# Kernel optimization log

Measured on AMD Instinct MI355X. Metric: run time of the kernel, lower is better.

## Reference

```python
import jax, jax.numpy as jnp
import numpy as np

N_NODES = 50000
N_EDGES = 800000
F_IN = 128
HIDDEN = 128
N_CLASSES = 10
N_GRAPHS = 256


def _glorot(key, shape):
    lim = float(np.sqrt(6.0 / (shape[0] + shape[1])))
    return jax.random.uniform(key, shape, jnp.float32, -lim, lim)


def setup_inputs() -> dict:
    key = jax.random.key(0)
    ks = jax.random.split(key, 12)
    x = jax.random.normal(ks[0], (N_NODES, F_IN), jnp.float32)
    edge_index = jax.random.randint(ks[1], (2, N_EDGES), 0, N_NODES, jnp.int64)
    batch = jnp.sort(jax.random.randint(ks[2], (N_NODES,), 0, N_GRAPHS, jnp.int64))
    dims = [(F_IN, HIDDEN), (HIDDEN, HIDDEN), (HIDDEN, N_CLASSES)]
    params = {}
    for i, (din, dout) in enumerate(dims, start=1):
        params[f"Wl{i}"] = _glorot(ks[2 + 2 * i], (din, dout))   # lin_l: applied to aggregated neighbors (has bias)
        params[f"bl{i}"] = jnp.zeros((dout,), jnp.float32)
        params[f"Wr{i}"] = _glorot(ks[3 + 2 * i], (din, dout))   # lin_r: applied to root/self features (no bias)
    return {"x": x, "edge_index": edge_index, "batch": batch, **params}


def _sage_conv(x, src, dst, Wl, bl, Wr):
    # mean aggregation of source features at destination nodes
    msg = x[src]                                                    # [E, D] gather
    ssum = jax.ops.segment_sum(msg, dst, num_segments=N_NODES)      # [N, D]
    cnt = jax.ops.segment_sum(jnp.ones((src.shape[0],), x.dtype), dst, num_segments=N_NODES)
    agg = ssum / jnp.maximum(cnt, 1.0)[:, None]
    return agg @ Wl + bl + x @ Wr


def reference(x, edge_index, batch, Wl1, bl1, Wr1, Wl2, bl2, Wr2, Wl3, bl3, Wr3):
    src, dst = edge_index[0], edge_index[1]
    h = _sage_conv(x, src, dst, Wl1, bl1, Wr1)
    h = _sage_conv(h, src, dst, Wl2, bl2, Wr2)
    h = _sage_conv(h, src, dst, Wl3, bl3, Wr3)                      # [N, C]
    # global mean pool over graphs
    gsum = jax.ops.segment_sum(h, batch, num_segments=N_GRAPHS)     # [G, C]
    gcnt = jax.ops.segment_sum(jnp.ones((h.shape[0],), h.dtype), batch, num_segments=N_GRAPHS)
    pooled = gsum / jnp.maximum(gcnt, 1.0)[:, None]
    return jax.nn.log_softmax(pooled, axis=-1)
```

## Files before the change

kernel.cpp:

```cpp
#include <hip/hip_runtime.h>


#define CAP 48
#define EB 4096

typedef __attribute__((ext_vector_type(8))) short short8;
typedef __attribute__((ext_vector_type(4))) float floatx4;

static __device__ __forceinline__ unsigned short f2bf(float f) {
    unsigned int u = __float_as_uint(f);
    u += 0x7FFFu + ((u >> 16) & 1u);
    return (unsigned short)(u >> 16);
}
static __device__ __forceinline__ float bf2f(unsigned short b) {
    return __uint_as_float(((unsigned int)b) << 16);
}
static __device__ __forceinline__ unsigned int packbf2(float a, float b) {
    return (unsigned int)f2bf(a) | ((unsigned int)f2bf(b) << 16);
}

__global__ void prep1(const int* __restrict__ ei, int E, int ablk, int nbk, int N,
                      unsigned int* __restrict__ bedges, int* __restrict__ runCnt,
                      const float* __restrict__ Wl2, const float* __restrict__ Wr2,
                      const float* __restrict__ Wl3, const float* __restrict__ Wr3,
                      float* __restrict__ m2Mg,
                      int* __restrict__ zero_base, int zero_words,
                      unsigned int* __restrict__ y3z, unsigned int* __restrict__ u1z,
                      unsigned int* __restrict__ u2w) {
    __shared__ int hist[512];
    __shared__ float wtT_s[128 * 20];
    if (blockIdx.x < (unsigned)ablk) {
        for (int i = threadIdx.x; i < nbk; i += 256) hist[i] = 0;
        __syncthreads();
        int e0 = blockIdx.x * EB + threadIdx.x;
        unsigned int pk[16];
        int bk[16], loc[16];
#pragma unroll
        for (int k = 0; k < 16; ++k) {
            int e = e0 + k * 256;
            if (e < E) {
                int src = ei[e];
                int dst = ei[E + e];
                bk[k] = dst >> 7;
                pk[k] = ((unsigned int)(dst & 127) << 16) | (unsigned int)src;
                loc[k] = atomicAdd(&hist[bk[k]], 1);
            } else bk[k] = -1;
        }
        __syncthreads();
        for (int i = threadIdx.x; i < nbk; i += 256)
            runCnt[(size_t)blockIdx.x * nbk + i] = hist[i];
#pragma unroll
        for (int k = 0; k < 16; ++k)
            if (bk[k] >= 0 && loc[k] < CAP)
                bedges[((size_t)bk[k] * ablk + blockIdx.x) * CAP + loc[k]] = pk[k];
        return;
    }
    int rb = blockIdx.x - ablk;
    if (rb < 4) {
        const int tid = threadIdx.x;
        for (int i = tid; i < 2560; i += 256) {
            int f = i / 20, c = i - f * 20;
            wtT_s[i] = (c < 10) ? Wl3[f * 10 + c] : Wr3[f * 10 + (c - 10)];
        }
        __syncthreads();
        int jl = tid >> 3;
        int cg = tid & 7;
        int j = rb * 32 + jl;
        const float* w2row = ((cg < 4) ? Wl2 : Wr2) + (size_t)j * 128;
        int c20 = (cg & 3) * 5;
        float acc[5] = {0.f, 0.f, 0.f, 0.f, 0.f};
        for (int f4 = 0; f4 < 32; ++f4) {
            float4 wv = *(const float4*)&w2row[f4 * 4];
#pragma unroll
            for (int e = 0; e < 4; ++e) {
                float w = (e == 0) ? wv.x : (e == 1) ? wv.y : (e == 2) ? wv.z : wv.w;
                const float* wt = &wtT_s[(f4 * 4 + e) * 20 + c20];
#pragma unroll
                for (int i = 0; i < 5; ++i) acc[i] += w * wt[i];
            }
        }
        int cc = (cg >> 2) * 20 + c20;
#pragma unroll
        for (int i = 0; i < 5; ++i) m2Mg[j * 40 + cc + i] = acc[i];
        return;
    }
    if (rb == 4) {
        if (threadIdx.x < 6)  y3z[(size_t)N * 6 + threadIdx.x] = 0;
        if (threadIdx.x >= 32 && threadIdx.x < 38)
            u1z[(size_t)N * 6 + (threadIdx.x - 32)] = 0;
        if (threadIdx.x >= 64 && threadIdx.x < 70)
            u2w[(size_t)N * 6 + (threadIdx.x - 64)] = 0;
        return;
    }
    int i = (rb - 5) * 256 + threadIdx.x;
    if (i < zero_words) zero_base[i] = 0;
}

__global__ __launch_bounds__(256) void prep2(
    const float* __restrict__ Wl1, const float* __restrict__ Wr1,
    const float* __restrict__ Wl3, const float* __restrict__ Wr3,
    const float* __restrict__ bl1, const float* __restrict__ bl2,
    const float* __restrict__ bl3,
    const float* __restrict__ m2Mg, short* __restrict__ Wq,
    float* __restrict__ cbv) {
    __shared__ float m2s[128 * 40];
    __shared__ float aLR[32][80];
    const int tid = threadIdx.x;
    if (blockIdx.x == 4) {
        for (int i = tid; i < 3072; i += 256) {
            int k = i & 127;
            int t = i >> 7;
            int mt = t / 6, m = 10 + t % 6;
            int ks = k >> 5, rem = k & 31, qq = rem >> 3, jj = rem & 7;
            int l = qq * 16 + m;
            Wq[(((mt * 4 + ks) * 64) + l) * 8 + jj] = 0;
        }
        if (tid < 30) {
            float s = 0.f;
            if (tid < 10) {
                int c = tid;
                for (int k = 0; k < 128; ++k) s += bl1[k] * m2Mg[k * 40 + c];
            } else if (tid < 20) {
                int c = tid - 10;
                for (int k = 0; k < 128; ++k)
                    s += bl1[k] * (m2Mg[k * 40 + 20 + c] + m2Mg[k * 40 + 10 + c]);
                for (int f = 0; f < 128; ++f) s += bl2[f] * Wl3[f * 10 + c];
            } else {
                int c = tid - 20;
                for (int k = 0; k < 128; ++k) s += bl1[k] * m2Mg[k * 40 + 30 + c];
                for (int f = 0; f < 128; ++f) s += bl2[f] * Wr3[f * 10 + c];
                s += bl3[c];
            }
            cbv[tid] = s;
        }
        return;
    }
    for (int i = tid; i < 5120; i += 256) m2s[i] = m2Mg[i];
    __syncthreads();
    int kl = tid >> 3;
    int cg = tid & 7;
    int k = blockIdx.x * 32 + kl;
    int c0 = cg * 5;
    const float* wl = Wl1 + (size_t)k * 128;
    const float* wr = Wr1 + (size_t)k * 128;
    float accL[5] = {0.f, 0.f, 0.f, 0.f, 0.f};
    float accR[5] = {0.f, 0.f, 0.f, 0.f, 0.f};
    for (int j4 = 0; j4 < 32; ++j4) {
        float4 wa = *(const float4*)&wl[j4 * 4];
        float4 wb = *(const float4*)&wr[j4 * 4];
#pragma unroll
        for (int e = 0; e < 4; ++e) {
            float wle = (e == 0) ? wa.x : (e == 1) ? wa.y : (e == 2) ? wa.z : wa.w;
            float wre = (e == 0) ? wb.x : (e == 1) ? wb.y : (e == 2) ? wb.z : wb.w;
            const float* mr = &m2s[(j4 * 4 + e) * 40 + c0];
#pragma unroll
            for (int i = 0; i < 5; ++i) {
                accL[i] += wle * mr[i];
                accR[i] += wre * mr[i];
            }
        }
    }
#pragma unroll
    for (int i = 0; i < 5; ++i) {
        aLR[kl][c0 + i] = accL[i];
        aLR[kl][40 + c0 + i] = accR[i];
    }
    __syncthreads();
    int ks = k >> 5, rem = k & 31, qq = rem >> 3, jj = rem & 7;
#pragma unroll
    for (int i = 0; i < 5; ++i) {
        int f = c0 + i;
        float val;
        if (f < 10) {
            val = aLR[kl][f];
        } else if (f < 20) {
            int c = f - 10;
            val = aLR[kl][40 + c] + aLR[kl][20 + c] + aLR[kl][10 + c];
        } else if (f < 30) {
            int c = f - 20;
            val = aLR[kl][40 + 10 + c] + aLR[kl][40 + 20 + c] + aLR[kl][30 + c];
        } else {
            int c = f - 30;
            val = aLR[kl][40 + 30 + c];
        }
        int mt = f / 10, c = f % 10;
        int l = qq * 16 + c;
        Wq[(((mt * 4 + ks) * 64) + l) * 8 + jj] = (short)f2bf(val);
    }
}

__global__ __launch_bounds__(256) void fillX(
    const float* __restrict__ x, const short* __restrict__ Wq,
    unsigned short* __restrict__ y3, float* __restrict__ yS, int N,
    int nbk, int ablk,
    const unsigned int* __restrict__ bedges, const int* __restrict__ runCnt,
    int* __restrict__ cnt, unsigned short* __restrict__ colbuf) {
    __shared__ unsigned short As[64 * 136];
    __shared__ int lcnt[128];
    if (blockIdx.x >= (unsigned)nbk) {
        int blk = blockIdx.x - nbk;
        int node0 = blk * 64;
#pragma unroll
        for (int c = 0; c < 8; ++c) {
            int idx = c * 256 + threadIdx.x;
            int r = idx >> 5;
            int c4 = idx & 31;
            int row = node0 + r;
            float4 v = make_float4(0.f, 0.f, 0.f, 0.f);
            if (row < N) v = *(const float4*)&x[(size_t)row * 128 + c4 * 4];
            ushort4 p;
            p.x = f2bf(v.x); p.y = f2bf(v.y); p.z = f2bf(v.z); p.w = f2bf(v.w);
            *(ushort4*)&As[r * 136 + c4 * 4] = p;
        }
        __syncthreads();

        const int w = threadIdx.x >> 6;
        const int lane = threadIdx.x & 63;
        const int q = lane >> 4;
        const int m = lane & 15;

        floatx4 acc[4] = {};
#pragma unroll
        for (int s = 0; s < 4; ++s) {
            short8 bfrag = *(const short8*)&As[(w * 16 + m) * 136 + s * 32 + q * 8];
#pragma unroll
            for (int mi = 0; mi < 4; ++mi) {
                short8 wf = *(const short8*)&Wq[((mi * 4 + s) * 64 + lane) * 8];
                acc[mi] = __builtin_amdgcn_mfma_f32_16x16x32_bf16(
                    wf, bfrag, acc[mi], 0, 0, 0);
            }
        }
        int node = node0 + w * 16 + m;
        if (node < N) {
            int l = q * 4;
            {
                floatx4 a = acc[0];
                if (l < 8) {
                    ushort4 p;
                    p.x = f2bf(a[0]); p.y = f2bf(a[1]);
                    p.z = f2bf(a[2]); p.w = f2bf(a[3]);
                    *(ushort4*)&y3[(size_t)node * 12 + l] = p;
                } else if (l == 8) {
                    ushort2 p2;
                    p2.x = f2bf(a[0]); p2.y = f2bf(a[1]);
                    *(ushort2*)&y3[(size_t)node * 12 + 8] = p2;
                }
            }
#pragma unroll
            for (int mi = 1; mi < 4; ++mi) {
                floatx4 a = acc[mi];
                size_t off = (size_t)node * 36 + (mi - 1) * 12 + l;
                if (l < 8) {
                    *(float4*)&yS[off] = make_float4(a[0], a[1], a[2], a[3]);
                } else if (l == 8) {
                    *(float2*)&yS[off] = make_float2(a[0], a[1]);
                }
            }
        }
    } else {
        int b = blockIdx.x;
        if (threadIdx.x < 128) lcnt[threadIdx.x] = 0;
        __syncthreads();
        for (int blk = threadIdx.x; blk < ablk; blk += 256) {
            int c = runCnt[(size_t)blk * nbk + b];
            c = min(c, CAP);
            size_t ebase = ((size_t)b * ablk + blk) * CAP;
            for (int i = 0; i < c; ++i) {
                unsigned int pk = bedges[ebase + i];
                int dl = pk >> 16;
                int slot = atomicAdd(&lcnt[dl], 1);
                if (slot < CAP)
                    colbuf[(size_t)(b * 128 + dl) * CAP + slot] =
                        (unsigned short)(pk & 0xFFFFu);
            }
        }
        __syncthreads();
        int node = b * 128 + threadIdx.x;
        if (threadIdx.x < 128 && node < N) cnt[node] = lcnt[threadIdx.x];
    }
}

__global__ __launch_bounds__(256) void g1(
    const unsigned int* __restrict__ y3z, const int* __restrict__ cnt,
    const unsigned short* __restrict__ colbuf, const float2* __restrict__ yS2,
    unsigned int* __restrict__ u1z, int N) {
    const int lane = threadIdx.x & 63;
    const int wvi = threadIdx.x >> 6;
    const int la = lane & 15;
    const int qb = lane & 48;
    const int node = blockIdx.x * 16 + wvi * 4 + (lane >> 4);
    const bool valid = node < N;
    const int nodec = valid ? node : N - 1;
    const int deg = cnt[nodec];
    const int d = valid ? min(deg, CAP) : 0;
    const unsigned short* cb = colbuf + (size_t)nodec * CAP;
    const int sub = (la < 5) ? la : la - 5;

    float f0 = 0.f, f1 = 0.f;
    int nb = (d + 15) >> 4;
    for (int b = 0; b < nb; ++b) {
        int slot = b * 16 + la;
        int idx = (slot < d) ? (int)cb[slot] : N;
        unsigned int vv[8];
#pragma unroll
        for (int j = 0; j < 8; ++j) {
            int s0 = __shfl(idx, qb + 2 * j, 64);
            int s1 = __shfl(idx, qb + 2 * j + 1, 64);
            int sr = (la < 5) ? s0 : s1;
            vv[j] = (la < 10) ? y3z[(size_t)sr * 6 + sub] : 0u;
        }
#pragma unroll
        for (int j = 0; j < 8; ++j) {
            f0 += bf2f((unsigned short)(vv[j] & 0xFFFF));
            f1 += bf2f((unsigned short)(vv[j] >> 16));
        }
    }
    int pl = (la < 5) ? (lane + 5) : (lane - 5);
    f0 += __shfl(f0, pl, 64);
    f1 += __shfl(f1, pl, 64);
    if (valid && la < 5) {
        float inv = 1.0f / (float)max(deg, 1);
        float2 sv = yS2[(size_t)node * 18 + la];
        u1z[(size_t)node * 6 + la] = packbf2(f0 * inv + sv.x, f1 * inv + sv.y);
    }
}

__global__ __launch_bounds__(256) void g2(
    const unsigned int* __restrict__ u1z, const int* __restrict__ cnt,
    const unsigned short* __restrict__ colbuf, const float2* __restrict__ yS2,
    const float2* __restrict__ cbv2, unsigned int* __restrict__ u2w, int N) {
    const int lane = threadIdx.x & 63;
    const int wvi = threadIdx.x >> 6;
    const int la = lane & 15;
    const int qb = lane & 48;
    const int node = blockIdx.x * 16 + wvi * 4 + (lane >> 4);
    const bool valid = node < N;
    const int nodec = valid ? node : N - 1;
    const int deg = cnt[nodec];
    const int d = valid ? min(deg, CAP) : 0;
    const unsigned short* cb = colbuf + (size_t)nodec * CAP;
    const int sub = (la < 5) ? la : la - 5;

    float f0 = 0.f, f1 = 0.f;
    int nb = (d + 15) >> 4;
    for (int b = 0; b < nb; ++b) {
        int slot = b * 16 + la;
        int idx = (slot < d) ? (int)cb[slot] : N;
        unsigned int vv[8];
#pragma unroll
        for (int j = 0; j < 8; ++j) {
            int s0 = __shfl(idx, qb + 2 * j, 64);
            int s1 = __shfl(idx, qb + 2 * j + 1, 64);
            int sr = (la < 5) ? s0 : s1;
            vv[j] = (la < 10) ? u1z[(size_t)sr * 6 + sub] : 0u;
        }
#pragma unroll
        for (int j = 0; j < 8; ++j) {
            f0 += bf2f((unsigned short)(vv[j] & 0xFFFF));
            f1 += bf2f((unsigned short)(vv[j] >> 16));
        }
    }
    int pl = (la < 5) ? (lane + 5) : (lane - 5);
    f0 += __shfl(f0, pl, 64);
    f1 += __shfl(f1, pl, 64);
    if (valid && la < 5) {
        float inv = 1.0f / (float)max(deg, 1);
        float2 sv = yS2[(size_t)node * 18 + 6 + la];
        float2 v1 = cbv2[la];
        float b0 = sv.x + ((deg > 0) ? v1.x : 0.f);
        float b1 = sv.y + ((deg > 0) ? v1.y : 0.f);
        u2w[(size_t)node * 6 + la] = packbf2(f0 * inv + b0, f1 * inv + b1);
    }
}

__global__ __launch_bounds__(256) void g3pool(
    const unsigned int* __restrict__ u2w, const int* __restrict__ cnt,
    const unsigned short* __restrict__ colbuf, const float2* __restrict__ yS2,
    const float2* __restrict__ cbv2, const int* __restrict__ batch,
    float* __restrict__ gsum, float* __restrict__ gcnt, int N) {
    __shared__ float ls[2816];
    for (int i = threadIdx.x; i < 2816; i += 256) ls[i] = 0.f;
    __syncthreads();

    const int lane = threadIdx.x & 63;
    const int wvi = threadIdx.x >> 6;
    const int la = lane & 15;
    const int qb = lane & 48;
    const int node = blockIdx.x * 16 + wvi * 4 + (lane >> 4);
    const bool valid = node < N;
    const int nodec = valid ? node : N - 1;
    const int deg = cnt[nodec];
    const int d = valid ? min(deg, CAP) : 0;
    const unsigned short* cb = colbuf + (size_t)nodec * CAP;
    const int sub = (la < 5) ? la : la - 5;

    float f0 = 0.f, f1 = 0.f;
    int nb = (d + 15) >> 4;
    for (int b = 0; b < nb; ++b) {
        int slot = b * 16 + la;
        int idx = (slot < d) ? (int)cb[slot] : N;
        unsigned int vv[8];
#pragma unroll
        for (int j = 0; j < 8; ++j) {
            int s0 = __shfl(idx, qb + 2 * j, 64);
            int s1 = __shfl(idx, qb + 2 * j + 1, 64);
            int sr = (la < 5) ? s0 : s1;
            vv[j] = (la < 10) ? u2w[(size_t)sr * 6 + sub] : 0u;
        }
#pragma unroll
        for (int j = 0; j < 8; ++j) {
            f0 += bf2f((unsigned short)(vv[j] & 0xFFFF));
            f1 += bf2f((unsigned short)(vv[j] >> 16));
        }
    }
    int pl = (la < 5) ? (lane + 5) : (lane - 5);
    f0 += __shfl(f0, pl, 64);
    f1 += __shfl(f1, pl, 64);
    if (valid && la < 5) {
        float inv = 1.0f / (float)max(deg, 1);
        float2 y0 = yS2[(size_t)node * 18 + 12 + la];
        float2 v0 = cbv2[5 + la];
        float2 vc = cbv2[10 + la];
        float h0 = f0 * inv + y0.x + ((deg > 0) ? v0.x : 0.f) + vc.x;
        float h1 = f1 * inv + y0.y + ((deg > 0) ? v0.y : 0.f) + vc.y;
        int g = batch[node];
        atomicAdd(&ls[g * 10 + 2 * la], h0);
        atomicAdd(&ls[g * 10 + 2 * la + 1], h1);
        if (la == 0) atomicAdd(&ls[2560 + g], 1.0f);
    }
    __syncthreads();
    for (int i = threadIdx.x; i < 2816; i += 256) {
        float v = ls[i];
        if (v != 0.f) {
            if (i < 2560) atomicAdd(&gsum[i], v);
            else          atomicAdd(&gcnt[i - 2560], v);
        }
    }
}

__global__ void finalize_pool(const float* __restrict__ gsum,
                              const float* __restrict__ gcnt,
                              float* __restrict__ out, int G) {
    int g = blockIdx.x * blockDim.x + threadIdx.x;
    if (g >= G) return;
    float inv = 1.0f / fmaxf(gcnt[g], 1.0f);
    float p[10];
    float m = -1e30f;
#pragma unroll
    for (int c = 0; c < 10; ++c) { p[c] = gsum[g * 10 + c] * inv; m = fmaxf(m, p[c]); }
    float s = 0.f;
#pragma unroll
    for (int c = 0; c < 10; ++c) s += expf(p[c] - m);
    float lse = logf(s);
#pragma unroll
    for (int c = 0; c < 10; ++c) out[g * 10 + c] = p[c] - m - lse;
}

extern "C" void kernel_launch(void* const* d_in, const int* in_sizes, int n_in,
                              void* d_out, int out_size, void* d_ws, size_t ws_size,
                              hipStream_t stream) {
    const float* x    = (const float*)d_in[0];
    const int*   ei   = (const int*)d_in[1];
    const int*   batch= (const int*)d_in[2];
    const float* Wl1  = (const float*)d_in[3];
    const float* bl1  = (const float*)d_in[4];
    const float* Wr1  = (const float*)d_in[5];
    const float* Wl2  = (const float*)d_in[6];
    const float* bl2  = (const float*)d_in[7];
    const float* Wr2  = (const float*)d_in[8];
    const float* Wl3  = (const float*)d_in[9];
    const float* bl3  = (const float*)d_in[10];
    const float* Wr3  = (const float*)d_in[11];
    float* out = (float*)d_out;

    const int N = in_sizes[2];
    const int E = in_sizes[1] / 2;
    const int G = out_size / 10;
    const int ablk = (E + EB - 1) / EB;
    const int nbk  = (N + 127) >> 7;

    char* ws = (char*)d_ws;
    size_t o = 0;
    float* gsum   = (float*)(ws + o); o += (size_t)G * 10 * 4;
    float* gcnt   = (float*)(ws + o); o += (size_t)G * 4;
    size_t zero_bytes = (o + 255) & ~(size_t)255;
    o = zero_bytes;
    int*            cnt    = (int*)(ws + o);            o += (size_t)N * 4;
    unsigned short* colbuf = (unsigned short*)(ws + o); o += ((size_t)N * CAP * 2 + 255) & ~(size_t)255;
    short*          Wq     = (short*)(ws + o);          o += (size_t)8192 * 2;
    float*          cbv    = (float*)(ws + o);          o += 32 * 4;
    o = (o + 255) & ~(size_t)255;
    float*          m2Mg   = (float*)(ws + o);          o += (size_t)128 * 40 * 4;
    o = (o + 255) & ~(size_t)255;
    unsigned short* y3t    = (unsigned short*)(ws + o); o += (size_t)(N + 1) * 12 * 2;
    o = (o + 255) & ~(size_t)255;
    float*          yS     = (float*)(ws + o);          o += (size_t)N * 36 * 4;
    unsigned short* u1z    = (unsigned short*)(ws + o); o += (size_t)(N + 1) * 12 * 2;
    o = (o + 255) & ~(size_t)255;
    unsigned short* u2w    = (unsigned short*)(ws + o); o += (size_t)(N + 1) * 12 * 2;
    o = (o + 255) & ~(size_t)255;
    unsigned int*   bedges = (unsigned int*)(ws + o);   o += (size_t)nbk * ablk * CAP * 4;
    int*            runCnt = (int*)(ws + o);            o += (size_t)ablk * nbk * 4;

    int zero_words = (int)(zero_bytes / 4);
    int zblocks = (zero_words + 255) / 256;
    prep1<<<ablk + 5 + zblocks, 256, 0, stream>>>(
        ei, E, ablk, nbk, N, bedges, runCnt,
        Wl2, Wr2, Wl3, Wr3, m2Mg,
        (int*)ws, zero_words,
        (unsigned int*)y3t, (unsigned int*)u1z, (unsigned int*)u2w);

    prep2<<<5, 256, 0, stream>>>(Wl1, Wr1, Wl3, Wr3, bl1, bl2, bl3,
                                 m2Mg, Wq, cbv);

    int gblocks = (N + 63) / 64;
    int ablocks = (N + 15) / 16;
    fillX<<<nbk + gblocks, 256, 0, stream>>>(x, Wq, y3t, yS, N,
                                             nbk, ablk, bedges, runCnt,
                                             cnt, colbuf);

    g1<<<ablocks, 256, 0, stream>>>((const unsigned int*)y3t, cnt, colbuf,
                                    (const float2*)yS, (unsigned int*)u1z, N);
    g2<<<ablocks, 256, 0, stream>>>((const unsigned int*)u1z, cnt, colbuf,
                                    (const float2*)yS, (const float2*)cbv,
                                    (unsigned int*)u2w, N);
    g3pool<<<ablocks, 256, 0, stream>>>((const unsigned int*)u2w, cnt, colbuf,
                                        (const float2*)yS, (const float2*)cbv,
                                        batch, gsum, gcnt, N);
    finalize_pool<<<1, 256, 0, stream>>>(gsum, gcnt, out, G);
}
```

Measured before the change: 170.0 us.

## Pad gathered bf16 rows to 16 elements and gather 8-byte chunks per lane

The per-node bf16 tables y3/u1/u2 are padded from 12 to 16 shorts (32 bytes), so each neighbour row is read as three uint2 loads. The gather loop now processes 4 neighbours per 16-lane group instead of 2 and reduces with xor shuffles. The loop over neighbours is fully unrolled over the CAP slots, with a per-chunk degree guard. This cuts the number of gather iterations and shuffles per edge, at the cost of 33% more table storage and padded writes in the producer and in the bias vector layout.

```diff
diff --git a/kernel.cpp b/kernel.cpp
--- a/kernel.cpp
+++ b/kernel.cpp
@@ -85,11 +85,11 @@
         return;
     }
     if (rb == 4) {
-        if (threadIdx.x < 6)  y3z[(size_t)N * 6 + threadIdx.x] = 0;
-        if (threadIdx.x >= 32 && threadIdx.x < 38)
-            u1z[(size_t)N * 6 + (threadIdx.x - 32)] = 0;
-        if (threadIdx.x >= 64 && threadIdx.x < 70)
-            u2w[(size_t)N * 6 + (threadIdx.x - 64)] = 0;
+        if (threadIdx.x < 8)  y3z[(size_t)N * 8 + threadIdx.x] = 0;
+        if (threadIdx.x >= 32 && threadIdx.x < 40)
+            u1z[(size_t)N * 8 + (threadIdx.x - 32)] = 0;
+        if (threadIdx.x >= 64 && threadIdx.x < 72)
+            u2w[(size_t)N * 8 + (threadIdx.x - 64)] = 0;
         return;
     }
     int i = (rb - 5) * 256 + threadIdx.x;
@@ -115,21 +115,22 @@
             int l = qq * 16 + m;
             Wq[(((mt * 4 + ks) * 64) + l) * 8 + jj] = 0;
         }
-        if (tid < 30) {
+        if (tid < 48) {
+            int grp = tid >> 4;
+            int c = tid & 15;
             float s = 0.f;
-            if (tid < 10) {
-                int c = tid;
-                for (int k = 0; k < 128; ++k) s += bl1[k] * m2Mg[k * 40 + c];
-            } else if (tid < 20) {
-                int c = tid - 10;
-                for (int k = 0; k < 128; ++k)
-                    s += bl1[k] * (m2Mg[k * 40 + 20 + c] + m2Mg[k * 40 + 10 + c]);
-                for (int f = 0; f < 128; ++f) s += bl2[f] * Wl3[f * 10 + c];
-            } else {
-                int c = tid - 20;
-                for (int k = 0; k < 128; ++k) s += bl1[k] * m2Mg[k * 40 + 30 + c];
-                for (int f = 0; f < 128; ++f) s += bl2[f] * Wr3[f * 10 + c];
-                s += bl3[c];
+            if (c < 10) {
+                if (grp == 0) {
+                    for (int k = 0; k < 128; ++k) s += bl1[k] * m2Mg[k * 40 + c];
+                } else if (grp == 1) {
+                    for (int k = 0; k < 128; ++k)
+                        s += bl1[k] * (m2Mg[k * 40 + 20 + c] + m2Mg[k * 40 + 10 + c]);
+                    for (int f = 0; f < 128; ++f) s += bl2[f] * Wl3[f * 10 + c];
+                } else {
+                    for (int k = 0; k < 128; ++k) s += bl1[k] * m2Mg[k * 40 + 30 + c];
+                    for (int f = 0; f < 128; ++f) s += bl2[f] * Wr3[f * 10 + c];
+                    s += bl3[c];
+                }
             }
             cbv[tid] = s;
         }
@@ -235,16 +236,10 @@
             int l = q * 4;
             {
                 floatx4 a = acc[0];
-                if (l < 8) {
-                    ushort4 p;
-                    p.x = f2bf(a[0]); p.y = f2bf(a[1]);
-                    p.z = f2bf(a[2]); p.w = f2bf(a[3]);
-                    *(ushort4*)&y3[(size_t)node * 12 + l] = p;
-                } else if (l == 8) {
-                    ushort2 p2;
-                    p2.x = f2bf(a[0]); p2.y = f2bf(a[1]);
-                    *(ushort2*)&y3[(size_t)node * 12 + 8] = p2;
-                }
+                ushort4 p;
+                p.x = f2bf(a[0]); p.y = f2bf(a[1]);
+                p.z = f2bf(a[2]); p.w = f2bf(a[3]);
+                *(ushort4*)&y3[(size_t)node * 16 + l] = p;
             }
 #pragma unroll
             for (int mi = 1; mi < 4; ++mi) {
@@ -253,7 +248,7 @@
                 if (l < 8) {
                     *(float4*)&yS[off] = make_float4(a[0], a[1], a[2], a[3]);
                 } else if (l == 8) {
-                    *(float2*)&yS[off] = make_float2(a[0], a[1]);
+                    *(float4*)&yS[off] = make_float4(a[0], a[1], a[2], a[3]);
                 }
             }
         }
@@ -280,103 +275,126 @@
     }
 }
 
+
 __global__ __launch_bounds__(256) void g1(
-    const unsigned int* __restrict__ y3z, const int* __restrict__ cnt,
-    const unsigned short* __restrict__ colbuf, const float2* __restrict__ yS2,
-    unsigned int* __restrict__ u1z, int N) {
+    const uint2* __restrict__ tbl, const int* __restrict__ cnt,
+    const unsigned short* __restrict__ colbuf, const float4* __restrict__ ySq,
+    uint2* __restrict__ outt, int N) {
     const int lane = threadIdx.x & 63;
     const int wvi = threadIdx.x >> 6;
     const int la = lane & 15;
     const int qb = lane & 48;
+    const int e = la >> 2;
+    const int p = la & 3;
     const int node = blockIdx.x * 16 + wvi * 4 + (lane >> 4);
     const bool valid = node < N;
     const int nodec = valid ? node : N - 1;
     const int deg = cnt[nodec];
     const int d = valid ? min(deg, CAP) : 0;
     const unsigned short* cb = colbuf + (size_t)nodec * CAP;
-    const int sub = (la < 5) ? la : la - 5;
-
-    float f0 = 0.f, f1 = 0.f;
-    int nb = (d + 15) >> 4;
-    for (int b = 0; b < nb; ++b) {
-        int slot = b * 16 + la;
-        int idx = (slot < d) ? (int)cb[slot] : N;
-        unsigned int vv[8];
-#pragma unroll
-        for (int j = 0; j < 8; ++j) {
-            int s0 = __shfl(idx, qb + 2 * j, 64);
-            int s1 = __shfl(idx, qb + 2 * j + 1, 64);
-            int sr = (la < 5) ? s0 : s1;
-            vv[j] = (la < 10) ? y3z[(size_t)sr * 6 + sub] : 0u;
-        }
-#pragma unroll
-        for (int j = 0; j < 8; ++j) {
-            f0 += bf2f((unsigned short)(vv[j] & 0xFFFF));
-            f1 += bf2f((unsigned short)(vv[j] >> 16));
-        }
-    }
-    int pl = (la < 5) ? (lane + 5) : (lane - 5);
-    f0 += __shfl(f0, pl, 64);
-    f1 += __shfl(f1, pl, 64);
-    if (valid && la < 5) {
-        float inv = 1.0f / (float)max(deg, 1);
-        float2 sv = yS2[(size_t)node * 18 + la];
-        u1z[(size_t)node * 6 + la] = packbf2(f0 * inv + sv.x, f1 * inv + sv.y);
+
+    int i0 = (la < d) ? (int)cb[la] : N;
+    int i1 = (16 + la < d) ? (int)cb[16 + la] : N;
+    int i2 = (32 + la < d) ? (int)cb[32 + la] : N;
+
+    float a0 = 0.f, a1 = 0.f, a2 = 0.f, a3 = 0.f;
+#pragma unroll
+    for (int k = 0; k < 3; ++k) {
+        int cur = (k == 0) ? i0 : ((k == 1) ? i1 : i2);
+#pragma unroll
+        for (int tt = 0; tt < 4; ++tt) {
+            int base = k * 16 + tt * 4;
+            if (base < d) {
+                int s = __shfl(cur, qb + tt * 4 + e, 64);
+                uint2 v = make_uint2(0u, 0u);
+                if (p < 3) v = tbl[(size_t)s * 4 + p];
+                a0 += bf2f((unsigned short)(v.x & 0xFFFF));
+                a1 += bf2f((unsigned short)(v.x >> 16));
+                a2 += bf2f((unsigned short)(v.y & 0xFFFF));
+                a3 += bf2f((unsigned short)(v.y >> 16));
+            }
+        }
+    }
+    a0 += __shfl_xor(a0, 4, 64); a0 += __shfl_xor(a0, 8, 64);
+    a1 += __shfl_xor(a1, 4, 64); a1 += __shfl_xor(a1, 8, 64);
+    a2 += __shfl_xor(a2, 4, 64); a2 += __shfl_xor(a2, 8, 64);
+    a3 += __shfl_xor(a3, 4, 64); a3 += __shfl_xor(a3, 8, 64);
+    if (valid && la < 4) {
+        uint2 o = make_uint2(0u, 0u);
+        if (la < 3) {
+            float inv = 1.0f / (float)max(deg, 1);
+            float4 sv = ySq[(size_t)node * 9 + la];
+            o.x = packbf2(a0 * inv + sv.x, a1 * inv + sv.y);
+            o.y = packbf2(a2 * inv + sv.z, a3 * inv + sv.w);
+        }
+        outt[(size_t)node * 4 + la] = o;
     }
 }
 
 __global__ __launch_bounds__(256) void g2(
-    const unsigned int* __restrict__ u1z, const int* __restrict__ cnt,
-    const unsigned short* __restrict__ colbuf, const float2* __restrict__ yS2,
-    const float2* __restrict__ cbv2, unsigned int* __restrict__ u2w, int N) {
+    const uint2* __restrict__ tbl, const int* __restrict__ cnt,
+    const unsigned short* __restrict__ colbuf, const float4* __restrict__ ySq,
+    const float* __restrict__ cbv, uint2* __restrict__ outt, int N) {
     const int lane = threadIdx.x & 63;
     const int wvi = threadIdx.x >> 6;
     const int la = lane & 15;
     const int qb = lane & 48;
+    const int e = la >> 2;
+    const int p = la & 3;
     const int node = blockIdx.x * 16 + wvi * 4 + (lane >> 4);
     const bool valid = node < N;
     const int nodec = valid ? node : N - 1;
     const int deg = cnt[nodec];
     const int d = valid ? min(deg, CAP) : 0;
     const unsigned short* cb = colbuf + (size_t)nodec * CAP;
-    const int sub = (la < 5) ? la : la - 5;
-
-    float f0 = 0.f, f1 = 0.f;
-    int nb = (d + 15) >> 4;
-    for (int b = 0; b < nb; ++b) {
-        int slot = b * 16 + la;
-        int idx = (slot < d) ? (int)cb[slot] : N;
-        unsigned int vv[8];
-#pragma unroll
-        for (int j = 0; j < 8; ++j) {
-            int s0 = __shfl(idx, qb + 2 * j, 64);
-            int s1 = __shfl(idx, qb + 2 * j + 1, 64);
-            int sr = (la < 5) ? s0 : s1;
-            vv[j] = (la < 10) ? u1z[(size_t)sr * 6 + sub] : 0u;
-        }
-#pragma unroll
-        for (int j = 0; j < 8; ++j) {
-            f0 += bf2f((unsigned short)(vv[j] & 0xFFFF));
-            f1 += bf2f((unsigned short)(vv[j] >> 16));
-        }
-    }
-    int pl = (la < 5) ? (lane + 5) : (lane - 5);
-    f0 += __shfl(f0, pl, 64);
-    f1 += __shfl(f1, pl, 64);
-    if (valid && la < 5) {
-        float inv = 1.0f / (float)max(deg, 1);
-        float2 sv = yS2[(size_t)node * 18 + 6 + la];
-        float2 v1 = cbv2[la];
-        float b0 = sv.x + ((deg > 0) ? v1.x : 0.f);
-        float b1 = sv.y + ((deg > 0) ? v1.y : 0.f);
-        u2w[(size_t)node * 6 + la] = packbf2(f0 * inv + b0, f1 * inv + b1);
+
+    int i0 = (la < d) ? (int)cb[la] : N;
+    int i1 = (16 + la < d) ? (int)cb[16 + la] : N;
+    int i2 = (32 + la < d) ? (int)cb[32 + la] : N;
+
+    float a0 = 0.f, a1 = 0.f, a2 = 0.f, a3 = 0.f;
+#pragma unroll
+    for (int k = 0; k < 3; ++k) {
+        int cur = (k == 0) ? i0 : ((k == 1) ? i1 : i2);
+#pragma unroll
+        for (int tt = 0; tt < 4; ++tt) {
+            int base = k * 16 + tt * 4;
+            if (base < d) {
+                int s = __shfl(cur, qb + tt * 4 + e, 64);
+                uint2 v = make_uint2(0u, 0u);
+                if (p < 3) v = tbl[(size_t)s * 4 + p];
+                a0 += bf2f((unsigned short)(v.x & 0xFFFF));
+                a1 += bf2f((unsigned short)(v.x >> 16));
+                a2 += bf2f((unsigned short)(v.y & 0xFFFF));
+                a3 += bf2f((unsigned short)(v.y >> 16));
+            }
+        }
+    }
+    a0 += __shfl_xor(a0, 4, 64); a0 += __shfl_xor(a0, 8, 64);
+    a1 += __shfl_xor(a1, 4, 64); a1 += __shfl_xor(a1, 8, 64);
+    a2 += __shfl_xor(a2, 4, 64); a2 += __shfl_xor(a2, 8, 64);
+    a3 += __shfl_xor(a3, 4, 64); a3 += __shfl_xor(a3, 8, 64);
+    if (valid && la < 4) {
+        uint2 o = make_uint2(0u, 0u);
+        if (la < 3) {
+            float inv = 1.0f / (float)max(deg, 1);
+            float4 sv = ySq[(size_t)node * 9 + 3 + la];
+            float4 v1 = *(const float4*)&cbv[la * 4];
+            float b0 = sv.x + ((deg > 0) ? v1.x : 0.f);
+            float b1 = sv.y + ((deg > 0) ? v1.y : 0.f);
+            float b2 = sv.z + ((deg > 0) ? v1.z : 0.f);
+            float b3 = sv.w + ((deg > 0) ? v1.w : 0.f);
+            o.x = packbf2(a0 * inv + b0, a1 * inv + b1);
+            o.y = packbf2(a2 * inv + b2, a3 * inv + b3);
+        }
+        outt[(size_t)node * 4 + la] = o;
     }
 }
 
 __global__ __launch_bounds__(256) void g3pool(
-    const unsigned int* __restrict__ u2w, const int* __restrict__ cnt,
-    const unsigned short* __restrict__ colbuf, const float2* __restrict__ yS2,
-    const float2* __restrict__ cbv2, const int* __restrict__ batch,
+    const uint2* __restrict__ tbl, const int* __restrict__ cnt,
+    const unsigned short* __restrict__ colbuf, const float4* __restrict__ ySq,
+    const float* __restrict__ cbv, const int* __restrict__ batch,
     float* __restrict__ gsum, float* __restrict__ gcnt, int N) {
     __shared__ float ls[2816];
     for (int i = threadIdx.x; i < 2816; i += 256) ls[i] = 0.f;
@@ -386,46 +404,58 @@
     const int wvi = threadIdx.x >> 6;
     const int la = lane & 15;
     const int qb = lane & 48;
+    const int e = la >> 2;
+    const int p = la & 3;
     const int node = blockIdx.x * 16 + wvi * 4 + (lane >> 4);
     const bool valid = node < N;
     const int nodec = valid ? node : N - 1;
     const int deg = cnt[nodec];
     const int d = valid ? min(deg, CAP) : 0;
     const unsigned short* cb = colbuf + (size_t)nodec * CAP;
-    const int sub = (la < 5) ? la : la - 5;
-
-    float f0 = 0.f, f1 = 0.f;
-    int nb = (d + 15) >> 4;
-    for (int b = 0; b < nb; ++b) {
-        int slot = b * 16 + la;
-        int idx = (slot < d) ? (int)cb[slot] : N;
-        unsigned int vv[8];
-#pragma unroll
-        for (int j = 0; j < 8; ++j) {
-            int s0 = __shfl(idx, qb + 2 * j, 64);
-            int s1 = __shfl(idx, qb + 2 * j + 1, 64);
-            int sr = (la < 5) ? s0 : s1;
-            vv[j] = (la < 10) ? u2w[(size_t)sr * 6 + sub] : 0u;
-        }
-#pragma unroll
-        for (int j = 0; j < 8; ++j) {
-            f0 += bf2f((unsigned short)(vv[j] & 0xFFFF));
-            f1 += bf2f((unsigned short)(vv[j] >> 16));
-        }
-    }
-    int pl = (la < 5) ? (lane + 5) : (lane - 5);
-    f0 += __shfl(f0, pl, 64);
-    f1 += __shfl(f1, pl, 64);
-    if (valid && la < 5) {
+
+    int i0 = (la < d) ? (int)cb[la] : N;
+    int i1 = (16 + la < d) ? (int)cb[16 + la] : N;
+    int i2 = (32 + la < d) ? (int)cb[32 + la] : N;
+
+    float a0 = 0.f, a1 = 0.f, a2 = 0.f, a3 = 0.f;
+#pragma unroll
+    for (int k = 0; k < 3; ++k) {
+        int cur = (k == 0) ? i0 : ((k == 1) ? i1 : i2);
+#pragma unroll
+        for (int tt = 0; tt < 4; ++tt) {
+            int base = k * 16 + tt * 4;
+            if (base < d) {
+                int s = __shfl(cur, qb + tt * 4 + e, 64);
+                uint2 v = make_uint2(0u, 0u);
+                if (p < 3) v = tbl[(size_t)s * 4 + p];
+                a0 += bf2f((unsigned short)(v.x & 0xFFFF));
+                a1 += bf2f((unsigned short)(v.x >> 16));
+                a2 += bf2f((unsigned short)(v.y & 0xFFFF));
+                a3 += bf2f((unsigned short)(v.y >> 16));
+            }
+        }
+    }
+    a0 += __shfl_xor(a0, 4, 64); a0 += __shfl_xor(a0, 8, 64);
+    a1 += __shfl_xor(a1, 4, 64); a1 += __shfl_xor(a1, 8, 64);
+    a2 += __shfl_xor(a2, 4, 64); a2 += __shfl_xor(a2, 8, 64);
+    a3 += __shfl_xor(a3, 4, 64); a3 += __shfl_xor(a3, 8, 64);
+    if (valid && la < 3) {
         float inv = 1.0f / (float)max(deg, 1);
-        float2 y0 = yS2[(size_t)node * 18 + 12 + la];
-        float2 v0 = cbv2[5 + la];
-        float2 vc = cbv2[10 + la];
-        float h0 = f0 * inv + y0.x + ((deg > 0) ? v0.x : 0.f) + vc.x;
-        float h1 = f1 * inv + y0.y + ((deg > 0) ? v0.y : 0.f) + vc.y;
+        float4 y0 = ySq[(size_t)node * 9 + 6 + la];
+        float4 v0 = *(const float4*)&cbv[16 + la * 4];
+        float4 vc = *(const float4*)&cbv[32 + la * 4];
+        float h0 = a0 * inv + y0.x + ((deg > 0) ? v0.x : 0.f) + vc.x;
+        float h1 = a1 * inv + y0.y + ((deg > 0) ? v0.y : 0.f) + vc.y;
+        float h2 = a2 * inv + y0.z + ((deg > 0) ? v0.z : 0.f) + vc.z;
+        float h3 = a3 * inv + y0.w + ((deg > 0) ? v0.w : 0.f) + vc.w;
         int g = batch[node];
-        atomicAdd(&ls[g * 10 + 2 * la], h0);
-        atomicAdd(&ls[g * 10 + 2 * la + 1], h1);
+        int c0 = la * 4;
+        atomicAdd(&ls[g * 10 + c0], h0);
+        atomicAdd(&ls[g * 10 + c0 + 1], h1);
+        if (la < 2) {
+            atomicAdd(&ls[g * 10 + c0 + 2], h2);
+            atomicAdd(&ls[g * 10 + c0 + 3], h3);
+        }
         if (la == 0) atomicAdd(&ls[2560 + g], 1.0f);
     }
     __syncthreads();
@@ -488,16 +518,17 @@
     int*            cnt    = (int*)(ws + o);            o += (size_t)N * 4;
     unsigned short* colbuf = (unsigned short*)(ws + o); o += ((size_t)N * CAP * 2 + 255) & ~(size_t)255;
     short*          Wq     = (short*)(ws + o);          o += (size_t)8192 * 2;
-    float*          cbv    = (float*)(ws + o);          o += 32 * 4;
+    float*          cbv    = (float*)(ws + o);          o += 48 * 4;
     o = (o + 255) & ~(size_t)255;
     float*          m2Mg   = (float*)(ws + o);          o += (size_t)128 * 40 * 4;
     o = (o + 255) & ~(size_t)255;
-    unsigned short* y3t    = (unsigned short*)(ws + o); o += (size_t)(N + 1) * 12 * 2;
+    unsigned short* y3t    = (unsigned short*)(ws + o); o += (size_t)(N + 1) * 16 * 2;
     o = (o + 255) & ~(size_t)255;
     float*          yS     = (float*)(ws + o);          o += (size_t)N * 36 * 4;
-    unsigned short* u1z    = (unsigned short*)(ws + o); o += (size_t)(N + 1) * 12 * 2;
     o = (o + 255) & ~(size_t)255;
-    unsigned short* u2w    = (unsigned short*)(ws + o); o += (size_t)(N + 1) * 12 * 2;
+    unsigned short* u1z    = (unsigned short*)(ws + o); o += (size_t)(N + 1) * 16 * 2;
+    o = (o + 255) & ~(size_t)255;
+    unsigned short* u2w    = (unsigned short*)(ws + o); o += (size_t)(N + 1) * 16 * 2;
     o = (o + 255) & ~(size_t)255;
     unsigned int*   bedges = (unsigned int*)(ws + o);   o += (size_t)nbk * ablk * CAP * 4;
     int*            runCnt = (int*)(ws + o);            o += (size_t)ablk * nbk * 4;
@@ -519,13 +550,12 @@
                                              nbk, ablk, bedges, runCnt,
                                              cnt, colbuf);
 
-    g1<<<ablocks, 256, 0, stream>>>((const unsigned int*)y3t, cnt, colbuf,
-                                    (const float2*)yS, (unsigned int*)u1z, N);
-    g2<<<ablocks, 256, 0, stream>>>((const unsigned int*)u1z, cnt, colbuf,
-                                    (const float2*)yS, (const float2*)cbv,
-                                    (unsigned int*)u2w, N);
-    g3pool<<<ablocks, 256, 0, stream>>>((const unsigned int*)u2w, cnt, colbuf,
-                                        (const float2*)yS, (const float2*)cbv,
+    g1<<<ablocks, 256, 0, stream>>>((const uint2*)y3t, cnt, colbuf,
+                                    (const float4*)yS, (uint2*)u1z, N);
+    g2<<<ablocks, 256, 0, stream>>>((const uint2*)u1z, cnt, colbuf,
+                                    (const float4*)yS, cbv, (uint2*)u2w, N);
+    g3pool<<<ablocks, 256, 0, stream>>>((const uint2*)u2w, cnt, colbuf,
+                                        (const float4*)yS, cbv,
                                         batch, gsum, gcnt, N);
     finalize_pool<<<1, 256, 0, stream>>>(gsum, gcnt, out, G);
 }
```

After: 170.0 us. No clear change (-0.0%).
